# Kernel optimization log

Measured on AMD Instinct MI355X. Metric: run time of the kernel, lower is better.

Reference implementation:

```python
import jax, jax.numpy as jnp
import numpy as np

B, S, D, H, FF = 2, 2048, 1024, 16, 4096
DH = D // H  # head dim


def _layernorm(x, g, b, eps=1e-5):
    m = x.mean(-1, keepdims=True)
    v = ((x - m) ** 2).mean(-1, keepdims=True)
    return (x - m) / jnp.sqrt(v + eps) * g + b


def setup_inputs() -> dict:
    key = jax.random.key(0)
    ks = jax.random.split(key, 10)
    s = 0.02
    return {
        "x": jax.random.normal(ks[0], (B, S, D), jnp.float32),
        "y": jax.random.normal(ks[1], (B, S, D), jnp.float32),
        "z": jax.random.normal(ks[2], (B, S, D), jnp.float32),
        "mask": jnp.ones((B, 1, S, S), jnp.int32),
        "Wq": jax.random.normal(ks[3], (D, D), jnp.float32) * s,
        "bq": jnp.zeros((D,), jnp.float32),
        "Wk": jax.random.normal(ks[4], (D, D), jnp.float32) * s,
        "bk": jnp.zeros((D,), jnp.float32),
        "Wv": jax.random.normal(ks[5], (D, D), jnp.float32) * s,
        "bv": jnp.zeros((D,), jnp.float32),
        "Wo": jax.random.normal(ks[6], (D, D), jnp.float32) * s,
        "bo": jnp.zeros((D,), jnp.float32),
        "W1": jax.random.normal(ks[7], (D, FF), jnp.float32) * s,
        "b1": jnp.zeros((FF,), jnp.float32),
        "W2": jax.random.normal(ks[8], (FF, D), jnp.float32) * s,
        "b2": jnp.zeros((D,), jnp.float32),
        "ln_g": jnp.ones((D,), jnp.float32),
        "ln_b": jnp.zeros((D,), jnp.float32),
    }


def reference(x, y, z, mask, Wq, bq, Wk, bk, Wv, bv, Wo, bo, W1, b1, W2, b2, ln_g, ln_b):
    q = (x @ Wq + bq).reshape(B, S, H, DH)
    k = (y @ Wk + bk).reshape(B, S, H, DH)
    v = (z @ Wv + bv).reshape(B, S, H, DH)
    # scores: [B, H, Q, K]
    scores = jnp.einsum('bqhl,bkhl->bhqk', q, k) / (DH ** 0.5)
    scores = jnp.where(mask == 0, jnp.float32(-1e10), scores)
    # NOTE: source softmaxes over dim=2 (the query axis) -- faithful.
    p = jax.nn.softmax(scores, axis=2)
    # Source einsum 'bhqk,bvhl->bvhl' sums p over q,k -> per-(b,h) scalar scaling v.
    s_bh = p.sum(axis=(2, 3))  # [B, H]
    att = s_bh[:, None, :, None] * v  # [B, S, H, DH]
    att = att.reshape(B, S, D) @ Wo + bo
    # shared AddAndNorm (same LayerNorm params used twice); dropout = identity (eval)
    h1 = _layernorm(z + att, ln_g, ln_b)
    ff = jax.nn.relu(h1 @ W1 + b1) @ W2 + b2
    return _layernorm(h1 + ff, ln_g, ln_b)
```

## Files before the change

### kernel.cpp

```cpp
#include <hip/hip_runtime.h>

static constexpr int kB = 2, kS = 2048, kD = 1024, kFF = 4096;
static constexpr int kM = kB * kS;
static constexpr size_t MB = 1u << 20;

typedef __attribute__((ext_vector_type(8))) short short8;
typedef __attribute__((ext_vector_type(4))) float f32x4;

__device__ __forceinline__ unsigned short f2bf(float f) {
  union { float f; unsigned int u; } c; c.f = f;
  unsigned int u = c.u;
  unsigned int r = u + 0x7FFFu + ((u >> 16) & 1u);
  return (unsigned short)(r >> 16);
}

__device__ __forceinline__ float bf2f(unsigned short b) {
  union { unsigned int u; float f; } c;
  c.u = ((unsigned int)b) << 16;
  return c.f;
}

__device__ __forceinline__ void gload_lds16(const void* g, void* l) {
  __builtin_amdgcn_global_load_lds(
      (const __attribute__((address_space(1))) void*)g,
      (__attribute__((address_space(3))) void*)l, 16, 0, 0);
}

__global__ __launch_bounds__(256) void cast_bf16_kernel(
    const float* __restrict__ in, unsigned short* __restrict__ out, int n) {
  int i = (blockIdx.x * 256 + threadIdx.x) * 4;
  if (i >= n) return;
  float4 v = *(const float4*)(in + i);
  ushort4 o;
  o.x = f2bf(v.x); o.y = f2bf(v.y); o.z = f2bf(v.z); o.w = f2bf(v.w);
  *(ushort4*)(out + i) = o;
}

__global__ __launch_bounds__(1024) void cast_transpose_kernel(
    const float* __restrict__ W, unsigned short* __restrict__ Wt,
    int K, int N, float scale) {
  __shared__ float tile[32][33];
  int nb = blockIdx.x * 32, kb = blockIdx.y * 32;
  int tx = threadIdx.x, ty = threadIdx.y;
  tile[ty][tx] = W[(size_t)(kb + ty) * N + (nb + tx)];
  __syncthreads();
  Wt[(size_t)(nb + ty) * K + (kb + tx)] = f2bf(tile[tx][ty] * scale);
}

__global__ __launch_bounds__(256) void bias_gemv_part_kernel(
    const float* __restrict__ bv, const float* __restrict__ Wo,
    float* __restrict__ partial) {
  const int b = blockIdx.x, t = threadIdx.x;
  const int c = t * 4;
  float4 acc = {0.f, 0.f, 0.f, 0.f};
#pragma unroll
  for (int r = 0; r < 8; ++r) {
    const int f = b * 8 + r;
    const float s = bv[f];
    float4 w = *(const float4*)(Wo + (size_t)f * 1024 + c);
    acc.x = fmaf(s, w.x, acc.x);
    acc.y = fmaf(s, w.y, acc.y);
    acc.z = fmaf(s, w.z, acc.z);
    acc.w = fmaf(s, w.w, acc.w);
  }
  *(float4*)(partial + (size_t)b * 1024 + c) = acc;
}

__global__ __launch_bounds__(256) void bias_gemv_fin_kernel(
    const float* __restrict__ partial, const float* __restrict__ bo,
    float* __restrict__ bc) {
  const int n = blockIdx.x * 256 + threadIdx.x;
  float acc = 0.0f;
#pragma unroll 8
  for (int b = 0; b < 128; ++b) acc += partial[(size_t)b * 1024 + n];
  bc[n] = 2048.0f * acc + bo[n];
}

__global__ __launch_bounds__(256) void combine_wc_kernel(
    const float* __restrict__ P, unsigned short* __restrict__ Wt) {
  const int i = (blockIdx.x * 256 + threadIdx.x) * 4;
  const int MN = 1024 * 1024;
  float4 s0 = *(const float4*)(P + i);
  float4 s1 = *(const float4*)(P + MN + i);
  float4 s2 = *(const float4*)(P + 2 * MN + i);
  float4 s3 = *(const float4*)(P + 3 * MN + i);
  const int row = i >> 10, col = i & 1023;
  float v0 = s0.x + s1.x + s2.x + s3.x + (row == col + 0 ? 1.0f : 0.0f);
  float v1 = s0.y + s1.y + s2.y + s3.y + (row == col + 1 ? 1.0f : 0.0f);
  float v2 = s0.z + s1.z + s2.z + s3.z + (row == col + 2 ? 1.0f : 0.0f);
  float v3 = s0.w + s1.w + s2.w + s3.w + (row == col + 3 ? 1.0f : 0.0f);
  ushort4 o; o.x = f2bf(v0); o.y = f2bf(v1); o.z = f2bf(v2); o.w = f2bf(v3);
  *(ushort4*)(Wt + i) = o;
}

template <int OUT_BF16, int RELU>
__global__ __launch_bounds__(256, 4) void gemm_bt(
    const unsigned short* __restrict__ A, const unsigned short* __restrict__ Bt,
    const float* __restrict__ bias, void* __restrict__ Cout,
    int M, int N, int K, int nXtiles, int nTilesPerSplit, int kSplitLen,
    size_t cStride, int cr, int cc) {
  __shared__ __align__(16) unsigned short sA[128 * 64];
  __shared__ __align__(16) unsigned short sB[128 * 64];
  const int tid = threadIdx.x;
  const int wave = tid >> 6, lane = tid & 63;
  const int wr = wave >> 1, wc = wave & 1;

  const int x = blockIdx.x & 7, j = blockIdx.x >> 3;
  const int bpc = cr * cc;
  const int chunkIdx = x + 8 * (j / bpc);
  const int w = j % bpc;
  const int chunksPerSplit = nTilesPerSplit / bpc;
  const int split = chunkIdx / chunksPerSplit;
  const int cL = chunkIdx % chunksPerSplit;
  const int cpr = nXtiles / cc;
  const int m0 = ((cL / cpr) * cr + w / cc) * 128;
  const int n0 = ((cL % cpr) * cc + w % cc) * 128;
  const int kBeg = split * kSplitLen, kEnd = kBeg + kSplitLen;

  const int srow = lane >> 3;
  const int scol = ((lane & 7) ^ srow) * 8;

  f32x4 acc[4][4] = {};

  for (int k0 = kBeg; k0 < kEnd; k0 += 64) {
#pragma unroll
    for (int i = 0; i < 4; ++i) {
      const int chunk = i * 4 + wave;
      const int rr = chunk * 8 + srow;
      gload_lds16(A + (size_t)(m0 + rr) * K + (k0 + scol), &sA[chunk * 512]);
      gload_lds16(Bt + (size_t)(n0 + rr) * K + (k0 + scol), &sB[chunk * 512]);
    }
    __syncthreads();
#pragma unroll
    for (int kk = 0; kk < 64; kk += 32) {
      const int kcol = kk + (lane >> 4) * 8;
      const int kswz = (lane & 7) * 8;
      short8 af[4], bfr[4];
#pragma unroll
      for (int m = 0; m < 4; ++m)
        af[m] = *(const short8*)&sA[(wr * 64 + m * 16 + (lane & 15)) * 64 + (kcol ^ kswz)];
#pragma unroll
      for (int n = 0; n < 4; ++n)
        bfr[n] = *(const short8*)&sB[(wc * 64 + n * 16 + (lane & 15)) * 64 + (kcol ^ kswz)];
#pragma unroll
      for (int m = 0; m < 4; ++m)
#pragma unroll
        for (int n = 0; n < 4; ++n)
          acc[m][n] = __builtin_amdgcn_mfma_f32_16x16x32_bf16(af[m], bfr[n], acc[m][n], 0, 0, 0);
    }
    __syncthreads();
  }

  const int cl = lane & 15, rg = lane >> 4;
  const float* bptr = (split == 0) ? bias : nullptr;
#pragma unroll
  for (int n = 0; n < 4; ++n) {
    const int col = n0 + wc * 64 + n * 16 + cl;
    const float bias_v = bptr ? bptr[col] : 0.0f;
#pragma unroll
    for (int m = 0; m < 4; ++m) {
      const int rbase = m0 + wr * 64 + m * 16 + rg * 4;
#pragma unroll
      for (int j2 = 0; j2 < 4; ++j2) {
        float v = acc[m][n][j2] + bias_v;
        if (RELU) v = fmaxf(v, 0.0f);
        const size_t idx = split * cStride + (size_t)(rbase + j2) * N + col;
        if (OUT_BF16)
          ((unsigned short*)Cout)[idx] = f2bf(v);
        else
          ((float*)Cout)[idx] = v;
      }
    }
  }
}

__global__ __launch_bounds__(256) void ln2_bf16_kernel(
    const unsigned short* __restrict__ P, size_t pStr,
    const float* __restrict__ gg, const float* __restrict__ bb,
    unsigned short* __restrict__ Hb) {
  const int row = blockIdx.x, t = threadIdx.x;
  const size_t base = (size_t)row * 1024 + t * 4;
  ushort4 v0 = *(const ushort4*)(P + base);
  ushort4 v1 = *(const ushort4*)(P + pStr + base);
  float a0 = bf2f(v0.x) + bf2f(v1.x);
  float a1 = bf2f(v0.y) + bf2f(v1.y);
  float a2 = bf2f(v0.z) + bf2f(v1.z);
  float a3 = bf2f(v0.w) + bf2f(v1.w);
  float s = a0 + a1 + a2 + a3;
  float ss = a0 * a0 + a1 * a1 + a2 * a2 + a3 * a3;
#pragma unroll
  for (int off = 32; off > 0; off >>= 1) {
    s += __shfl_down(s, off);
    ss += __shfl_down(ss, off);
  }
  __shared__ float rs[4], rss[4];
  __shared__ float smean, srstd;
  const int wave = t >> 6, lane = t & 63;
  if (lane == 0) { rs[wave] = s; rss[wave] = ss; }
  __syncthreads();
  if (t == 0) {
    float S1 = rs[0] + rs[1] + rs[2] + rs[3];
    float S2 = rss[0] + rss[1] + rss[2] + rss[3];
    float mean = S1 * (1.0f / 1024.0f);
    float var = S2 * (1.0f / 1024.0f) - mean * mean;
    smean = mean;
    srstd = rsqrtf(var + 1e-5f);
  }
  __syncthreads();
  const float mean = smean, rstd = srstd;
  float4 gv = *(const float4*)(gg + t * 4);
  float4 bv = *(const float4*)(bb + t * 4);
  ushort4 hb;
  hb.x = f2bf((a0 - mean) * rstd * gv.x + bv.x);
  hb.y = f2bf((a1 - mean) * rstd * gv.y + bv.y);
  hb.z = f2bf((a2 - mean) * rstd * gv.z + bv.z);
  hb.w = f2bf((a3 - mean) * rstd * gv.w + bv.w);
  *(ushort4*)(Hb + base) = hb;
}

__global__ __launch_bounds__(256) void ln_fin4_kernel(
    const unsigned short* __restrict__ Res, const unsigned short* __restrict__ P,
    size_t pStr, const float* __restrict__ gg, const float* __restrict__ bb,
    float* __restrict__ out) {
  const int row = blockIdx.x, t = threadIdx.x;
  const size_t base = (size_t)row * 1024 + t * 4;
  ushort4 rv = *(const ushort4*)(Res + base);
  ushort4 v0 = *(const ushort4*)(P + base);
  ushort4 v1 = *(const ushort4*)(P + pStr + base);
  ushort4 v2 = *(const ushort4*)(P + 2 * pStr + base);
  ushort4 v3 = *(const ushort4*)(P + 3 * pStr + base);
  float a0 = bf2f(rv.x) + bf2f(v0.x) + bf2f(v1.x) + bf2f(v2.x) + bf2f(v3.x);
  float a1 = bf2f(rv.y) + bf2f(v0.y) + bf2f(v1.y) + bf2f(v2.y) + bf2f(v3.y);
  float a2 = bf2f(rv.z) + bf2f(v0.z) + bf2f(v1.z) + bf2f(v2.z) + bf2f(v3.z);
  float a3 = bf2f(rv.w) + bf2f(v0.w) + bf2f(v1.w) + bf2f(v2.w) + bf2f(v3.w);
  float s = a0 + a1 + a2 + a3;
  float ss = a0 * a0 + a1 * a1 + a2 * a2 + a3 * a3;
#pragma unroll
  for (int off = 32; off > 0; off >>= 1) {
    s += __shfl_down(s, off);
    ss += __shfl_down(ss, off);
  }
  __shared__ float rs[4], rss[4];
  __shared__ float smean, srstd;
  const int wave = t >> 6, lane = t & 63;
  if (lane == 0) { rs[wave] = s; rss[wave] = ss; }
  __syncthreads();
  if (t == 0) {
    float S1 = rs[0] + rs[1] + rs[2] + rs[3];
    float S2 = rss[0] + rss[1] + rss[2] + rss[3];
    float mean = S1 * (1.0f / 1024.0f);
    float var = S2 * (1.0f / 1024.0f) - mean * mean;
    smean = mean;
    srstd = rsqrtf(var + 1e-5f);
  }
  __syncthreads();
  const float mean = smean, rstd = srstd;
  float4 gv = *(const float4*)(gg + t * 4);
  float4 bv = *(const float4*)(bb + t * 4);
  float4 ov;
  ov.x = (a0 - mean) * rstd * gv.x + bv.x;
  ov.y = (a1 - mean) * rstd * gv.y + bv.y;
  ov.z = (a2 - mean) * rstd * gv.z + bv.z;
  ov.w = (a3 - mean) * rstd * gv.w + bv.w;
  *(float4*)(out + base) = ov;
}

extern "C" void kernel_launch(void* const* d_in, const int* in_sizes, int n_in,
                              void* d_out, int out_size, void* d_ws, size_t ws_size,
                              hipStream_t stream) {
  const float* z  = (const float*)d_in[2];
  const float* Wv = (const float*)d_in[8];
  const float* bv = (const float*)d_in[9];
  const float* Wo = (const float*)d_in[10];
  const float* bo = (const float*)d_in[11];
  const float* W1 = (const float*)d_in[12];
  const float* b1 = (const float*)d_in[13];
  const float* W2 = (const float*)d_in[14];
  const float* b2 = (const float*)d_in[15];
  const float* lng = (const float*)d_in[16];
  const float* lnb = (const float*)d_in[17];
  float* out = (float*)d_out;

  char* ws = (char*)d_ws;
  unsigned short* zbf  = (unsigned short*)(ws + 0 * MB);
  unsigned short* a1   = (unsigned short*)(ws + 0 * MB);
  float*          wcp  = (float*)(ws + 32 * MB);
  unsigned short* attP = (unsigned short*)(ws + 32 * MB);
  unsigned short* ffP  = (unsigned short*)(ws + 32 * MB);
  unsigned short* h1bf = (unsigned short*)(ws + 96 * MB);
  unsigned short* WoT  = (unsigned short*)(ws + 104 * MB);
  unsigned short* WvBf = (unsigned short*)(ws + 106 * MB);
  unsigned short* WcT  = (unsigned short*)(ws + 108 * MB);
  float*          bc   = (float*)(ws + 110 * MB);
  float*          bprt = (float*)(ws + 110 * MB + 65536);
  unsigned short* wT   = (unsigned short*)(ws + 104 * MB);

  const int nZ = kM * kD;
  const size_t pStr = (size_t)kM * kD;

  cast_transpose_kernel<<<dim3(kD / 32, kD / 32), dim3(32, 32), 0, stream>>>(
      Wo, WoT, kD, kD, (float)kS);
  cast_bf16_kernel<<<dim3(kD * kD / 1024), dim3(256), 0, stream>>>(Wv, WvBf, kD * kD);
  bias_gemv_part_kernel<<<dim3(128), dim3(256), 0, stream>>>(bv, Wo, bprt);
  bias_gemv_fin_kernel<<<dim3(4), dim3(256), 0, stream>>>(bprt, bo, bc);
  cast_bf16_kernel<<<dim3(nZ / 1024), dim3(256), 0, stream>>>(z, zbf, nZ);

  gemm_bt<0, 0><<<dim3(256), dim3(256), 0, stream>>>(
      WoT, WvBf, nullptr, wcp, kD, kD, kD, kD / 128, 64, 256, (size_t)kD * kD,
      8, 4);
  combine_wc_kernel<<<dim3(1024), dim3(256), 0, stream>>>(wcp, WcT);

  gemm_bt<1, 0><<<dim3(512), dim3(256), 0, stream>>>(
      zbf, WcT, bc, attP, kM, kD, kD, kD / 128, 256, 512, pStr, 8, 8);

  ln2_bf16_kernel<<<dim3(kM), dim3(256), 0, stream>>>(attP, pStr, lng, lnb, h1bf);

  cast_transpose_kernel<<<dim3(kFF / 32, kD / 32), dim3(32, 32), 0, stream>>>(
      W1, wT, kD, kFF, 1.0f);
  gemm_bt<1, 1><<<dim3(1024), dim3(256), 0, stream>>>(
      h1bf, wT, b1, a1, kM, kFF, kD, kFF / 128, 1024, kD, 0, 16, 8);

  cast_transpose_kernel<<<dim3(kD / 32, kFF / 32), dim3(32, 32), 0, stream>>>(
      W2, wT, kFF, kD, 1.0f);
  gemm_bt<1, 0><<<dim3(1024), dim3(256), 0, stream>>>(
      a1, wT, b2, ffP, kM, kD, kFF, kD / 128, 256, kFF / 4, pStr, 16, 8);

  ln_fin4_kernel<<<dim3(kM), dim3(256), 0, stream>>>(h1bf, ffP, pStr, lng, lnb, out);
}
```

Baseline: 165.8 us.

## Fuse z cast into GEMM, drop split-K weight combine, widen transposes

The fp32-to-bf16 cast of z moves into the attention GEMM's A-tile load through registers, so the separate cast kernel and its bf16 round trip go away. The Wo·Wv weight-combine GEMM now runs without split-K (64 blocks) and adds the identity in its epilogue, which removes the fp32 partial buffer and the combine kernel. The cast-transpose kernels switch to 64x64 tiles with float4 loads and ushort4 stores, and W1T/W2T get separate buffers. In exchange, the fused A path gives up the async global-to-LDS load, and the 64-block weight GEMM leaves much of the GPU idle.

New measurement: 163.7 us. About the same (-1.3%).

```diff
diff --git a/kernel.cpp b/kernel.cpp
--- a/kernel.cpp
+++ b/kernel.cpp
@@ -36,15 +36,33 @@
   *(ushort4*)(out + i) = o;
 }
 
-__global__ __launch_bounds__(1024) void cast_transpose_kernel(
+__global__ __launch_bounds__(256) void cast_transpose64(
     const float* __restrict__ W, unsigned short* __restrict__ Wt,
-    int K, int N, float scale) {
-  __shared__ float tile[32][33];
-  int nb = blockIdx.x * 32, kb = blockIdx.y * 32;
-  int tx = threadIdx.x, ty = threadIdx.y;
-  tile[ty][tx] = W[(size_t)(kb + ty) * N + (nb + tx)];
-  __syncthreads();
-  Wt[(size_t)(nb + ty) * K + (kb + tx)] = f2bf(tile[tx][ty] * scale);
+    int K, int N, float scale, int ntN) {
+  __shared__ float tile[64][65];
+  const int bid = blockIdx.x;
+  const int nb = (bid % ntN) * 64, kb = (bid / ntN) * 64;
+  const int tx = threadIdx.x & 15, ty = threadIdx.x >> 4;
+#pragma unroll
+  for (int p = 0; p < 4; ++p) {
+    const int r = ty + 16 * p;
+    float4 v = *(const float4*)(W + (size_t)(kb + r) * N + nb + tx * 4);
+    tile[r][tx * 4 + 0] = v.x;
+    tile[r][tx * 4 + 1] = v.y;
+    tile[r][tx * 4 + 2] = v.z;
+    tile[r][tx * 4 + 3] = v.w;
+  }
+  __syncthreads();
+#pragma unroll
+  for (int p = 0; p < 4; ++p) {
+    const int n = ty + 16 * p;
+    ushort4 o;
+    o.x = f2bf(tile[tx * 4 + 0][n] * scale);
+    o.y = f2bf(tile[tx * 4 + 1][n] * scale);
+    o.z = f2bf(tile[tx * 4 + 2][n] * scale);
+    o.w = f2bf(tile[tx * 4 + 3][n] * scale);
+    *(ushort4*)(Wt + (size_t)(nb + n) * K + kb + tx * 4) = o;
+  }
 }
 
 __global__ __launch_bounds__(256) void bias_gemv_part_kernel(
@@ -76,31 +94,16 @@
   bc[n] = 2048.0f * acc + bo[n];
 }
 
-__global__ __launch_bounds__(256) void combine_wc_kernel(
-    const float* __restrict__ P, unsigned short* __restrict__ Wt) {
-  const int i = (blockIdx.x * 256 + threadIdx.x) * 4;
-  const int MN = 1024 * 1024;
-  float4 s0 = *(const float4*)(P + i);
-  float4 s1 = *(const float4*)(P + MN + i);
-  float4 s2 = *(const float4*)(P + 2 * MN + i);
-  float4 s3 = *(const float4*)(P + 3 * MN + i);
-  const int row = i >> 10, col = i & 1023;
-  float v0 = s0.x + s1.x + s2.x + s3.x + (row == col + 0 ? 1.0f : 0.0f);
-  float v1 = s0.y + s1.y + s2.y + s3.y + (row == col + 1 ? 1.0f : 0.0f);
-  float v2 = s0.z + s1.z + s2.z + s3.z + (row == col + 2 ? 1.0f : 0.0f);
-  float v3 = s0.w + s1.w + s2.w + s3.w + (row == col + 3 ? 1.0f : 0.0f);
-  ushort4 o; o.x = f2bf(v0); o.y = f2bf(v1); o.z = f2bf(v2); o.w = f2bf(v3);
-  *(ushort4*)(Wt + i) = o;
-}
-
-template <int OUT_BF16, int RELU>
+template <int OUT_BF16, int RELU, int ADD_I, int A_F32>
 __global__ __launch_bounds__(256, 4) void gemm_bt(
-    const unsigned short* __restrict__ A, const unsigned short* __restrict__ Bt,
+    const void* __restrict__ A, const unsigned short* __restrict__ Bt,
     const float* __restrict__ bias, void* __restrict__ Cout,
     int M, int N, int K, int nXtiles, int nTilesPerSplit, int kSplitLen,
     size_t cStride, int cr, int cc) {
   __shared__ __align__(16) unsigned short sA[128 * 64];
   __shared__ __align__(16) unsigned short sB[128 * 64];
+  const unsigned short* Ab = (const unsigned short*)A;
+  const float* Af = (const float*)A;
   const int tid = threadIdx.x;
   const int wave = tid >> 6, lane = tid & 63;
   const int wr = wave >> 1, wc = wave & 1;
@@ -123,11 +126,38 @@
   f32x4 acc[4][4] = {};
 
   for (int k0 = kBeg; k0 < kEnd; k0 += 64) {
+    if constexpr (A_F32) {
+      float4 pa[4][2];
+#pragma unroll
+      for (int i = 0; i < 4; ++i) {
+        const int chunk = i * 4 + wave;
+        const int rr = chunk * 8 + srow;
+        const float* az = Af + (size_t)(m0 + rr) * K + (k0 + scol);
+        pa[i][0] = *(const float4*)az;
+        pa[i][1] = *(const float4*)(az + 4);
+      }
+#pragma unroll
+      for (int i = 0; i < 4; ++i) {
+        const int chunk = i * 4 + wave;
+        short8 cv;
+        cv[0] = (short)f2bf(pa[i][0].x); cv[1] = (short)f2bf(pa[i][0].y);
+        cv[2] = (short)f2bf(pa[i][0].z); cv[3] = (short)f2bf(pa[i][0].w);
+        cv[4] = (short)f2bf(pa[i][1].x); cv[5] = (short)f2bf(pa[i][1].y);
+        cv[6] = (short)f2bf(pa[i][1].z); cv[7] = (short)f2bf(pa[i][1].w);
+        *(short8*)&sA[chunk * 512 + lane * 8] = cv;
+      }
+    } else {
+#pragma unroll
+      for (int i = 0; i < 4; ++i) {
+        const int chunk = i * 4 + wave;
+        const int rr = chunk * 8 + srow;
+        gload_lds16(Ab + (size_t)(m0 + rr) * K + (k0 + scol), &sA[chunk * 512]);
+      }
+    }
 #pragma unroll
     for (int i = 0; i < 4; ++i) {
       const int chunk = i * 4 + wave;
       const int rr = chunk * 8 + srow;
-      gload_lds16(A + (size_t)(m0 + rr) * K + (k0 + scol), &sA[chunk * 512]);
       gload_lds16(Bt + (size_t)(n0 + rr) * K + (k0 + scol), &sB[chunk * 512]);
     }
     __syncthreads();
@@ -163,6 +193,7 @@
 #pragma unroll
       for (int j2 = 0; j2 < 4; ++j2) {
         float v = acc[m][n][j2] + bias_v;
+        if (ADD_I && (rbase + j2 == col)) v += 1.0f;
         if (RELU) v = fmaxf(v, 0.0f);
         const size_t idx = split * cStride + (size_t)(rbase + j2) * N + col;
         if (OUT_BF16)
@@ -282,48 +313,43 @@
   float* out = (float*)d_out;
 
   char* ws = (char*)d_ws;
-  unsigned short* zbf  = (unsigned short*)(ws + 0 * MB);
   unsigned short* a1   = (unsigned short*)(ws + 0 * MB);
-  float*          wcp  = (float*)(ws + 32 * MB);
   unsigned short* attP = (unsigned short*)(ws + 32 * MB);
   unsigned short* ffP  = (unsigned short*)(ws + 32 * MB);
+  unsigned short* W2T  = (unsigned short*)(ws + 64 * MB);
+  unsigned short* WoT  = (unsigned short*)(ws + 88 * MB);
+  unsigned short* WvBf = (unsigned short*)(ws + 90 * MB);
+  unsigned short* WcT  = (unsigned short*)(ws + 92 * MB);
+  float*          bc   = (float*)(ws + 94 * MB);
+  float*          bprt = (float*)(ws + 94 * MB + 65536);
   unsigned short* h1bf = (unsigned short*)(ws + 96 * MB);
-  unsigned short* WoT  = (unsigned short*)(ws + 104 * MB);
-  unsigned short* WvBf = (unsigned short*)(ws + 106 * MB);
-  unsigned short* WcT  = (unsigned short*)(ws + 108 * MB);
-  float*          bc   = (float*)(ws + 110 * MB);
-  float*          bprt = (float*)(ws + 110 * MB + 65536);
-  unsigned short* wT   = (unsigned short*)(ws + 104 * MB);
-
-  const int nZ = kM * kD;
+  unsigned short* W1T  = (unsigned short*)(ws + 104 * MB);
+
   const size_t pStr = (size_t)kM * kD;
 
-  cast_transpose_kernel<<<dim3(kD / 32, kD / 32), dim3(32, 32), 0, stream>>>(
-      Wo, WoT, kD, kD, (float)kS);
+  cast_transpose64<<<dim3(256), dim3(256), 0, stream>>>(
+      Wo, WoT, kD, kD, (float)kS, kD / 64);
   cast_bf16_kernel<<<dim3(kD * kD / 1024), dim3(256), 0, stream>>>(Wv, WvBf, kD * kD);
   bias_gemv_part_kernel<<<dim3(128), dim3(256), 0, stream>>>(bv, Wo, bprt);
   bias_gemv_fin_kernel<<<dim3(4), dim3(256), 0, stream>>>(bprt, bo, bc);
-  cast_bf16_kernel<<<dim3(nZ / 1024), dim3(256), 0, stream>>>(z, zbf, nZ);
-
-  gemm_bt<0, 0><<<dim3(256), dim3(256), 0, stream>>>(
-      WoT, WvBf, nullptr, wcp, kD, kD, kD, kD / 128, 64, 256, (size_t)kD * kD,
-      8, 4);
-  combine_wc_kernel<<<dim3(1024), dim3(256), 0, stream>>>(wcp, WcT);
-
-  gemm_bt<1, 0><<<dim3(512), dim3(256), 0, stream>>>(
-      zbf, WcT, bc, attP, kM, kD, kD, kD / 128, 256, 512, pStr, 8, 8);
+
+  gemm_bt<1, 0, 1, 0><<<dim3(64), dim3(256), 0, stream>>>(
+      WoT, WvBf, nullptr, WcT, kD, kD, kD, kD / 128, 64, kD, 0, 4, 2);
+
+  gemm_bt<1, 0, 0, 1><<<dim3(512), dim3(256), 0, stream>>>(
+      z, WcT, bc, attP, kM, kD, kD, kD / 128, 256, 512, pStr, 8, 8);
 
   ln2_bf16_kernel<<<dim3(kM), dim3(256), 0, stream>>>(attP, pStr, lng, lnb, h1bf);
 
-  cast_transpose_kernel<<<dim3(kFF / 32, kD / 32), dim3(32, 32), 0, stream>>>(
-      W1, wT, kD, kFF, 1.0f);
-  gemm_bt<1, 1><<<dim3(1024), dim3(256), 0, stream>>>(
-      h1bf, wT, b1, a1, kM, kFF, kD, kFF / 128, 1024, kD, 0, 16, 8);
-
-  cast_transpose_kernel<<<dim3(kD / 32, kFF / 32), dim3(32, 32), 0, stream>>>(
-      W2, wT, kFF, kD, 1.0f);
-  gemm_bt<1, 0><<<dim3(1024), dim3(256), 0, stream>>>(
-      a1, wT, b2, ffP, kM, kD, kFF, kD / 128, 256, kFF / 4, pStr, 16, 8);
+  cast_transpose64<<<dim3(1024), dim3(256), 0, stream>>>(
+      W1, W1T, kD, kFF, 1.0f, kFF / 64);
+  gemm_bt<1, 1, 0, 0><<<dim3(1024), dim3(256), 0, stream>>>(
+      h1bf, W1T, b1, a1, kM, kFF, kD, kFF / 128, 1024, kD, 0, 16, 8);
+
+  cast_transpose64<<<dim3(1024), dim3(256), 0, stream>>>(
+      W2, W2T, kFF, kD, 1.0f, kD / 64);
+  gemm_bt<1, 0, 0, 0><<<dim3(1024), dim3(256), 0, stream>>>(
+      a1, W2T, b2, ffP, kM, kD, kFF, kD / 128, 256, kFF / 4, pStr, 16, 8);
 
   ln_fin4_kernel<<<dim3(kM), dim3(256), 0, stream>>>(h1bf, ffP, pStr, lng, lnb, out);
 }
```
